# Performance work log

Hardware: AMD Instinct MI355X
Metric: run time of the kernel (lower is better)

Reference implementation:

```python
import jax, jax.numpy as jnp
import numpy as np

BN_EPS = 1e-5
TAU = 1.0

def _conv(x, w, pad, groups=1):
    return jax.lax.conv_general_dilated(
        x, w, (1, 1), [(pad, pad), (pad, pad)],
        feature_group_count=groups,
        dimension_numbers=('NCHW', 'OIHW', 'NCHW'))

def _bn(x, p):
    # p: (4, C) rows = gamma, beta, running_mean, running_var (eval-mode BN)
    g, b, m, v = p[0], p[1], p[2], p[3]
    scale = g * jax.lax.rsqrt(v + BN_EPS)
    shift = b - m * scale
    return x * scale[None, :, None, None] + shift[None, :, None, None]

def _dsconv(x, dw, bn1, pw, bn2, pad):
    c = x.shape[1]
    h = jax.nn.silu(_bn(_conv(x, dw, pad, groups=c), bn1))
    return jax.nn.silu(_bn(_conv(h, pw, 0), bn2))

def _make_bn(key, ch):
    k1, k2, k3, k4 = jax.random.split(key, 4)
    g = 1.0 + 0.1 * jax.random.normal(k1, (ch,), jnp.float32)
    b = 0.1 * jax.random.normal(k2, (ch,), jnp.float32)
    m = 0.1 * jax.random.normal(k3, (ch,), jnp.float32)
    v = 0.5 + jax.random.uniform(k4, (ch,), jnp.float32)
    return jnp.stack([g, b, m, v])

def setup_inputs() -> dict:
    key = jax.random.key(0)
    ks = jax.random.split(key, 18)
    B, C, H, W = 4, 256, 128, 128
    P, K = 64, 8
    inp = {
        'x':      jax.random.normal(ks[0], (B, C, H, W), jnp.float32),
        'fp_w1':  0.05 * jax.random.normal(ks[1], (P, C, 1, 1), jnp.float32),
        'fp_bn1': _make_bn(ks[2], P),
        'fp_dw':  0.2 * jax.random.normal(ks[3], (P, 1, 3, 3), jnp.float32),
        'fp_bn2': _make_bn(ks[4], P),
        'protos': jax.random.normal(ks[5], (K, P), jnp.float32),
        'bs_dw':  0.2 * jax.random.normal(ks[6], (1, 1, 3, 3), jnp.float32),
        'bs_bn1': _make_bn(ks[7], 1),
        'bs_pw':  0.2 * jax.random.normal(ks[8], (8, 1, 1, 1), jnp.float32),
        'bs_bn2': _make_bn(ks[9], 8),
        'bl_dw':  0.2 * jax.random.normal(ks[10], (1, 1, 5, 5), jnp.float32),
        'bl_bn1': _make_bn(ks[11], 1),
        'bl_pw':  0.2 * jax.random.normal(ks[12], (8, 1, 1, 1), jnp.float32),
        'bl_bn2': _make_bn(ks[13], 8),
        'fuse_w': 0.2 * jax.random.normal(ks[14], (1, 16, 1, 1), jnp.float32),
        'fuse_b': 0.1 * jax.random.normal(ks[15], (1,), jnp.float32),
        'gamma':  0.5 * jax.random.normal(ks[16], (1,), jnp.float32),
    }
    return inp

def reference(x, fp_w1, fp_bn1, fp_dw, fp_bn2, protos,
              bs_dw, bs_bn1, bs_pw, bs_bn2,
              bl_dw, bl_bn1, bl_pw, bl_bn2,
              fuse_w, fuse_b, gamma):
    # feature_proj: 1x1 conv -> BN -> SiLU -> depthwise 3x3 -> BN -> SiLU
    h = jax.nn.silu(_bn(_conv(x, fp_w1, 0), fp_bn1))
    proj = jax.nn.silu(_bn(_conv(h, fp_dw, 1, groups=fp_dw.shape[0]), fp_bn2))

    # deviation: min L2 distance to K bg prototypes, per-image min-max normalized
    B, P, H, W = proj.shape
    feat = proj.reshape(B, P, H * W).transpose(0, 2, 1)      # (B, HW, P)
    d2 = ((feat * feat).sum(-1, keepdims=True)               # (B, HW, 1)
          + (protos * protos).sum(-1)                        # (K,)
          - 2.0 * jnp.einsum('bnp,kp->bnk', feat, protos))   # (B, HW, K)
    dist = jnp.sqrt(jnp.maximum(d2, 0.0))
    min_dist = dist.min(axis=2) / (TAU + 1e-6)               # (B, HW)
    d_min = min_dist.min(axis=1, keepdims=True)
    d_max = min_dist.max(axis=1, keepdims=True)
    deviation = ((min_dist - d_min) / (d_max - d_min + 1e-6)).reshape(B, 1, H, W)

    # deviation -> attention head: two DS-conv branches (3x3 and 5x5), fuse 1x1, sigmoid
    f1 = _dsconv(deviation, bs_dw, bs_bn1, bs_pw, bs_bn2, pad=1)
    f2 = _dsconv(deviation, bl_dw, bl_bn1, bl_pw, bl_bn2, pad=2)
    attn = jax.nn.sigmoid(_conv(jnp.concatenate([f1, f2], axis=1), fuse_w, 0)
                          + fuse_b[None, :, None, None])
    return x + gamma * (x * attn)
```

## Files before the change

### kernel.cpp

```cpp
#include <hip/hip_runtime.h>
#include <math.h>

#define C_IN 256
#define P_CH 64
#define H_IMG 128
#define W_IMG 128
#define HW (H_IMG*W_IMG)
#define N_IMG 4
#define K_PROTO 8
#define BN_EPS 1e-5f

typedef unsigned short u16;
typedef __attribute__((ext_vector_type(4))) short bf16x4;
typedef __attribute__((ext_vector_type(8))) short bf16x8;
typedef __attribute__((ext_vector_type(4))) float f32x4;

#define OFF_WTBF   0
#define OFF_BIASA  8192
#define OFF_PNORM  8256
#define OFF_MINMAX 8264
#define OFF_H      8272
#define OFF_MD     (8272 + 2097152)
#define OFF_ATTN   (OFF_MD + 65536)

__device__ __forceinline__ float silu_f(float x) { return x / (1.f + __expf(-x)); }

__device__ __forceinline__ u16 f2bf(float f) {
    union { float f; unsigned u; } v; v.f = f;
    unsigned r = v.u + 0x7fffu + ((v.u >> 16) & 1u);
    return (u16)(r >> 16);
}
__device__ __forceinline__ float bf2f(u16 s) {
    union { unsigned u; float f; } v; v.u = ((unsigned)s) << 16; return v.f;
}

__global__ void prep_kernel(const float* __restrict__ w1, const float* __restrict__ bn1,
                            const float* __restrict__ protos, float* __restrict__ ws)
{
    int bx = blockIdx.x, tid = threadIdx.x;
    if (bx < 64) {
        int idx = bx * 256 + tid;
        int n = idx >> 8, k = idx & 255;
        float sc = bn1[n] * rsqrtf(bn1[192 + n] + BN_EPS);
        ((u16*)(ws + OFF_WTBF))[idx] = f2bf(w1[n * C_IN + k] * sc);
    } else {
        if (tid < 64) {
            float sc = bn1[tid] * rsqrtf(bn1[192 + tid] + BN_EPS);
            ws[OFF_BIASA + tid] = bn1[64 + tid] - bn1[128 + tid] * sc;
        }
        if (tid < 8) {
            float s = 0.f;
            for (int p = 0; p < 64; ++p) { float v = protos[tid * 64 + p]; s += v * v; }
            ws[OFF_PNORM + tid] = s;
        }
        if (tid < 4) {
            unsigned* mm = (unsigned*)(ws + OFF_MINMAX);
            mm[tid * 2]     = 0x7f7fffffu;
            mm[tid * 2 + 1] = 0u;
        }
    }
}

#define LDA 36
#define LDB 264
__global__ __launch_bounds__(256) void conv1x1_kernel(
    const float* __restrict__ x, const u16* __restrict__ wtb,
    const float* __restrict__ bias, u16* __restrict__ h)
{
    __shared__ u16 As[2][128 * LDA];
    __shared__ u16 Bs[64 * LDB];
    int bx = blockIdx.x;
    int img = bx >> 7, row = bx & 127;
    int tid = threadIdx.x;
    int wid = tid >> 6, lane = tid & 63;
    int mm = lane & 15, kb = lane >> 4;

    {
        int n = tid >> 2, k0 = (tid & 3) * 64;
        const u16* src = wtb + n * 256 + k0;
        u16* dst = Bs + n * LDB + k0;
#pragma unroll
        for (int i = 0; i < 64; i += 4)
            *(ushort4*)(dst + i) = *(const ushort4*)(src + i);
    }

    int cp = tid >> 4, pg = tid & 15;
    const float* xbase = x + (size_t)img * C_IN * HW + row * W_IMG;
    {
        const float* xc0 = xbase + (size_t)(2 * cp) * HW;
        const float* xc1 = xc0 + HW;
#pragma unroll
        for (int i = 0; i < 8; ++i) {
            int px = pg + 16 * i;
            ushort2 pk; pk.x = f2bf(xc0[px]); pk.y = f2bf(xc1[px]);
            *(ushort2*)(&As[0][px * LDA + 2 * cp]) = pk;
        }
    }
    __syncthreads();

    f32x4 acc[2][4];
#pragma unroll
    for (int mt = 0; mt < 2; ++mt)
#pragma unroll
        for (int nt = 0; nt < 4; ++nt) acc[mt][nt] = (f32x4){0.f, 0.f, 0.f, 0.f};

    for (int k = 0; k < 8; ++k) {
        float p0[8], p1[8];
        if (k < 7) {
            const float* xc0 = xbase + (size_t)((k + 1) * 32 + 2 * cp) * HW;
            const float* xc1 = xc0 + HW;
#pragma unroll
            for (int i = 0; i < 8; ++i) {
                int px = pg + 16 * i;
                p0[i] = xc0[px]; p1[i] = xc1[px];
            }
        }

        const u16* Ab = As[k & 1];
        bf16x8 afrag[2], bfrag[4];
#pragma unroll
        for (int mt = 0; mt < 2; ++mt) {
            const u16* ap = Ab + (wid * 32 + mt * 16 + mm) * LDA + kb * 8;
            bf16x4 lo = *(const bf16x4*)ap;
            bf16x4 hi = *(const bf16x4*)(ap + 4);
            afrag[mt] = __builtin_shufflevector(lo, hi, 0, 1, 2, 3, 4, 5, 6, 7);
        }
#pragma unroll
        for (int nt = 0; nt < 4; ++nt)
            bfrag[nt] = *(const bf16x8*)(Bs + (nt * 16 + mm) * LDB + k * 32 + kb * 8);
#pragma unroll
        for (int mt = 0; mt < 2; ++mt)
#pragma unroll
            for (int nt = 0; nt < 4; ++nt)
                acc[mt][nt] = __builtin_amdgcn_mfma_f32_16x16x32_bf16(
                    afrag[mt], bfrag[nt], acc[mt][nt], 0, 0, 0);

        if (k < 7) {
            u16* An = As[(k + 1) & 1];
#pragma unroll
            for (int i = 0; i < 8; ++i) {
                int px = pg + 16 * i;
                ushort2 pk; pk.x = f2bf(p0[i]); pk.y = f2bf(p1[i]);
                *(ushort2*)(&An[px * LDA + 2 * cp]) = pk;
            }
        }
        __syncthreads();
    }

#pragma unroll
    for (int mt = 0; mt < 2; ++mt) {
        int pxb = wid * 32 + mt * 16 + kb * 4;
#pragma unroll
        for (int nt = 0; nt < 4; ++nt) {
            int n = nt * 16 + mm;
            float bb = bias[n];
            ushort4 o;
            o.x = f2bf(silu_f(acc[mt][nt][0] + bb));
            o.y = f2bf(silu_f(acc[mt][nt][1] + bb));
            o.z = f2bf(silu_f(acc[mt][nt][2] + bb));
            o.w = f2bf(silu_f(acc[mt][nt][3] + bb));
            *(ushort4*)(h + ((size_t)img * P_CH + n) * HW + row * W_IMG + pxb) = o;
        }
    }
}

__global__ __launch_bounds__(1024) void dwconv_dev_kernel(
    const u16* __restrict__ h, const float* __restrict__ dw,
    const float* __restrict__ bn2, const float* __restrict__ protos,
    const float* __restrict__ pnorm, float* __restrict__ md,
    unsigned* __restrict__ minmax)
{
    __shared__ float smem[4 * 8 * 324];
    int img = blockIdx.x >> 6;
    int t = blockIdx.x & 63;
    int y0 = (t >> 3) << 4, x0 = (t & 7) << 4;
    int tid = threadIdx.x;
    int q = tid >> 8;
    int qtid = tid & 255;
    int ty = qtid >> 4, tx = qtid & 15;

    const u16* himg = h + (size_t)img * P_CH * HW;
    float* qt = smem + q * (8 * 324);

    int  pre_off[11];
    bool pre_ok[11];
    bool pre_v[11];
#pragma unroll
    for (int r = 0; r < 11; ++r) {
        int l = qtid + r * 256;
        bool valid = l < 2592;
        int cl = l / 324;
        int rr = l - cl * 324;
        int ly = rr / 18, lx = rr - ly * 18;
        int yy = y0 - 1 + ly, xx = x0 - 1 + lx;
        bool inb = (yy >= 0) & (yy < H_IMG) & (xx >= 0) & (xx < W_IMG);
        pre_v[r] = valid;
        pre_ok[r] = valid && inb;
        pre_off[r] = cl * HW + (inb ? (yy * W_IMG + xx) : 0);
    }

    float norm2 = 0.f;
    float dot[K_PROTO];
#pragma unroll
    for (int k = 0; k < K_PROTO; ++k) dot[k] = 0.f;

    {
        const u16* hs = himg + (size_t)(q * 16) * HW;
#pragma unroll
        for (int r = 0; r < 11; ++r) {
            float v = pre_ok[r] ? bf2f(hs[pre_off[r]]) : 0.f;
            if (pre_v[r]) qt[qtid + r * 256] = v;
        }
    }
    __syncthreads();

    for (int k = 0; k < 2; ++k) {
        float pf[11];
        if (k == 0) {
            const u16* hs = himg + (size_t)(q * 16 + 8) * HW;
#pragma unroll
            for (int r = 0; r < 11; ++r)
                pf[r] = pre_ok[r] ? bf2f(hs[pre_off[r]]) : 0.f;
        }

        int c0 = q * 16 + k * 8;
#pragma unroll
        for (int cl = 0; cl < 8; ++cl) {
            int ch = c0 + cl;
            const float* tc = qt + cl * 324;
            const float* wch = dw + ch * 9;
            float s = 0.f;
#pragma unroll
            for (int dy = 0; dy < 3; ++dy)
#pragma unroll
                for (int dx = 0; dx < 3; ++dx)
                    s = fmaf(tc[(ty + dy) * 18 + tx + dx], wch[dy * 3 + dx], s);
            float g = bn2[ch], bb = bn2[64 + ch], m = bn2[128 + ch], vv = bn2[192 + ch];
            float scale = g * rsqrtf(vv + BN_EPS);
            float val = silu_f(scale * s + (bb - m * scale));
            norm2 = fmaf(val, val, norm2);
#pragma unroll
            for (int kk = 0; kk < K_PROTO; ++kk)
                dot[kk] = fmaf(val, protos[kk * 64 + ch], dot[kk]);
        }

        if (k == 0) {
            __syncthreads();
#pragma unroll
            for (int r = 0; r < 11; ++r)
                if (pre_v[r]) qt[qtid + r * 256] = pf[r];
            __syncthreads();
        }
    }
    __syncthreads();

    float* P = smem;
    {
        float* dst = P + (q * 256 + qtid) * 9;
        dst[0] = norm2;
#pragma unroll
        for (int kk = 0; kk < K_PROTO; ++kk) dst[1 + kk] = dot[kk];
    }
    __syncthreads();

    float wmin = 1e30f, wmax = -1e30f, mdv = 0.f;
    if (q == 0) {
        float n2 = 0.f, dd[K_PROTO];
#pragma unroll
        for (int kk = 0; kk < K_PROTO; ++kk) dd[kk] = 0.f;
#pragma unroll
        for (int qq = 0; qq < 4; ++qq) {
            const float* src = P + (qq * 256 + qtid) * 9;
            n2 += src[0];
#pragma unroll
            for (int kk = 0; kk < K_PROTO; ++kk) dd[kk] += src[1 + kk];
        }
        float d2min = 1e30f;
#pragma unroll
        for (int kk = 0; kk < K_PROTO; ++kk)
            d2min = fminf(d2min, n2 + pnorm[kk] - 2.f * dd[kk]);
        mdv = sqrtf(fmaxf(d2min, 0.f)) * (1.f / 1.000001f);
        md[img * HW + (y0 + ty) * W_IMG + (x0 + tx)] = mdv;
        wmin = mdv; wmax = mdv;
#pragma unroll
        for (int d = 32; d > 0; d >>= 1) {
            wmin = fminf(wmin, __shfl_xor(wmin, d));
            wmax = fmaxf(wmax, __shfl_xor(wmax, d));
        }
    }
    __syncthreads();
    if (q == 0 && (qtid & 63) == 0) {
        int wid = qtid >> 6;
        smem[wid * 2]     = wmin;
        smem[wid * 2 + 1] = wmax;
    }
    __syncthreads();
    if (tid == 0) {
        float bmin = fminf(fminf(smem[0], smem[2]), fminf(smem[4], smem[6]));
        float bmax = fmaxf(fmaxf(smem[1], smem[3]), fmaxf(smem[5], smem[7]));
        atomicMin(&minmax[img * 2],     __float_as_uint(bmin));
        atomicMax(&minmax[img * 2 + 1], __float_as_uint(bmax));
    }
}

__global__ __launch_bounds__(256) void attn_kernel(
    const float* __restrict__ md, const unsigned* __restrict__ minmax,
    const float* __restrict__ bs_dw, const float* __restrict__ bs_bn1,
    const float* __restrict__ bs_pw, const float* __restrict__ bs_bn2,
    const float* __restrict__ bl_dw, const float* __restrict__ bl_bn1,
    const float* __restrict__ bl_pw, const float* __restrict__ bl_bn2,
    const float* __restrict__ fuse_w, const float* __restrict__ fuse_b,
    float* __restrict__ attn)
{
    __shared__ float tile[20 * 20];
    int img = blockIdx.x >> 6;
    int t = blockIdx.x & 63;
    int y0 = (t >> 3) << 4, x0 = (t & 7) << 4;
    int tid = threadIdx.x;
    int ty = tid >> 4, tx = tid & 15;

    float fdmin = __uint_as_float(minmax[img * 2]);
    float fdmax = __uint_as_float(minmax[img * 2 + 1]);
    float inv = 1.f / (fdmax - fdmin + 1e-6f);

    const float* mdi = md + img * HW;
    for (int l = tid; l < 400; l += 256) {
        int ly = l / 20, lx = l - ly * 20;
        int yy = y0 - 2 + ly, xx = x0 - 2 + lx;
        float v = 0.f;
        if (yy >= 0 && yy < H_IMG && xx >= 0 && xx < W_IMG)
            v = (mdi[yy * W_IMG + xx] - fdmin) * inv;
        tile[l] = v;
    }
    __syncthreads();

    float c3 = 0.f;
#pragma unroll
    for (int dy = 0; dy < 3; ++dy)
#pragma unroll
        for (int dx = 0; dx < 3; ++dx)
            c3 = fmaf(tile[(ty + 1 + dy) * 20 + tx + 1 + dx], bs_dw[dy * 3 + dx], c3);
    float c5 = 0.f;
#pragma unroll
    for (int dy = 0; dy < 5; ++dy)
#pragma unroll
        for (int dx = 0; dx < 5; ++dx)
            c5 = fmaf(tile[(ty + dy) * 20 + tx + dx], bl_dw[dy * 5 + dx], c5);

    float s1 = bs_bn1[0] * rsqrtf(bs_bn1[3] + BN_EPS);
    float t1 = silu_f(s1 * c3 + (bs_bn1[1] - bs_bn1[2] * s1));
    float s2 = bl_bn1[0] * rsqrtf(bl_bn1[3] + BN_EPS);
    float t2 = silu_f(s2 * c5 + (bl_bn1[1] - bl_bn1[2] * s2));

    float acc = fuse_b[0];
#pragma unroll
    for (int c = 0; c < 8; ++c) {
        float scs = bs_bn2[c] * rsqrtf(bs_bn2[24 + c] + BN_EPS);
        float u1 = silu_f(scs * (bs_pw[c] * t1) + (bs_bn2[8 + c] - bs_bn2[16 + c] * scs));
        acc = fmaf(fuse_w[c], u1, acc);
        float scl = bl_bn2[c] * rsqrtf(bl_bn2[24 + c] + BN_EPS);
        float u2 = silu_f(scl * (bl_pw[c] * t2) + (bl_bn2[8 + c] - bl_bn2[16 + c] * scl));
        acc = fmaf(fuse_w[8 + c], u2, acc);
    }
    float a = 1.f / (1.f + __expf(-acc));
    attn[img * HW + (y0 + ty) * W_IMG + (x0 + tx)] = a;
}

__global__ __launch_bounds__(256) void final_kernel(
    const float* __restrict__ x, const float* __restrict__ attn,
    const float* __restrict__ gamma, float* __restrict__ out)
{
    size_t i = ((size_t)blockIdx.x * 256 + (size_t)threadIdx.x) * 4;
    float g = gamma[0];
    int b = (int)(i / ((size_t)C_IN * HW));
    int hw = (int)(i % HW);
    const float4 xv = *(const float4*)(x + i);
    const float4 av = *(const float4*)(attn + (size_t)b * HW + hw);
    float4 o;
    o.x = xv.x * (1.f + g * av.x);
    o.y = xv.y * (1.f + g * av.y);
    o.z = xv.z * (1.f + g * av.z);
    o.w = xv.w * (1.f + g * av.w);
    *(float4*)(out + i) = o;
}

extern "C" void kernel_launch(void* const* d_in, const int* in_sizes, int n_in,
                              void* d_out, int out_size, void* d_ws, size_t ws_size,
                              hipStream_t stream) {
    const float* x      = (const float*)d_in[0];
    const float* fp_w1  = (const float*)d_in[1];
    const float* fp_bn1 = (const float*)d_in[2];
    const float* fp_dw  = (const float*)d_in[3];
    const float* fp_bn2 = (const float*)d_in[4];
    const float* protos = (const float*)d_in[5];
    const float* bs_dw  = (const float*)d_in[6];
    const float* bs_bn1 = (const float*)d_in[7];
    const float* bs_pw  = (const float*)d_in[8];
    const float* bs_bn2 = (const float*)d_in[9];
    const float* bl_dw  = (const float*)d_in[10];
    const float* bl_bn1 = (const float*)d_in[11];
    const float* bl_pw  = (const float*)d_in[12];
    const float* bl_bn2 = (const float*)d_in[13];
    const float* fuse_w = (const float*)d_in[14];
    const float* fuse_b = (const float*)d_in[15];
    const float* gamma  = (const float*)d_in[16];
    float* ws  = (float*)d_ws;
    float* out = (float*)d_out;

    prep_kernel<<<65, 256, 0, stream>>>(fp_w1, fp_bn1, protos, ws);
    conv1x1_kernel<<<512, 256, 0, stream>>>(x, (const u16*)(ws + OFF_WTBF),
                                            ws + OFF_BIASA, (u16*)(ws + OFF_H));
    dwconv_dev_kernel<<<256, 1024, 0, stream>>>((const u16*)(ws + OFF_H), fp_dw, fp_bn2,
                                                protos, ws + OFF_PNORM, ws + OFF_MD,
                                                (unsigned*)(ws + OFF_MINMAX));
    attn_kernel<<<256, 256, 0, stream>>>(ws + OFF_MD, (const unsigned*)(ws + OFF_MINMAX),
                                         bs_dw, bs_bn1, bs_pw, bs_bn2,
                                         bl_dw, bl_bn1, bl_pw, bl_bn2,
                                         fuse_w, fuse_b, ws + OFF_ATTN);
    final_kernel<<<16384, 256, 0, stream>>>(x, ws + OFF_ATTN, gamma, out);
}
```

Before: 188.9 us.

## Fuse 1x1 conv GEMM with depthwise conv and prototype distance via halo tiles

Merges the bf16 MFMA 1x1 projection and the depthwise 3x3 + prototype-distance kernels into one kernel that works on 16x8 pixel tiles with a one-pixel halo. The projected features stay in shared memory, so the intermediate h tensor is no longer written to and read back from global memory. The cost is recomputing the GEMM on halo pixels (180 of 192 padded rows per tile for 128 outputs) and more gather-like loads of x with boundary masks. A-tile double buffering is dropped in favour of a single buffer with extra barriers, and min/max reductions are adjusted to the new tile layout.

After: 221.5 us. +17.3%, slower.

```diff
diff --git a/kernel.cpp b/kernel.cpp
--- a/kernel.cpp
+++ b/kernel.cpp
@@ -19,8 +19,7 @@
 #define OFF_BIASA  8192
 #define OFF_PNORM  8256
 #define OFF_MINMAX 8264
-#define OFF_H      8272
-#define OFF_MD     (8272 + 2097152)
+#define OFF_MD     8272
 #define OFF_ATTN   (OFF_MD + 65536)
 
 __device__ __forceinline__ float silu_f(float x) { return x / (1.f + __expf(-x)); }
@@ -61,16 +60,30 @@
     }
 }
 
-#define LDA 36
-#define LDB 264
-__global__ __launch_bounds__(256) void conv1x1_kernel(
+#define HALO_PX 180
+#define M_PAD   192
+#define LDA     36
+#define LDB     264
+#define LDH     200
+__global__ __launch_bounds__(256, 2) void fused_front_kernel(
     const float* __restrict__ x, const u16* __restrict__ wtb,
-    const float* __restrict__ bias, u16* __restrict__ h)
+    const float* __restrict__ biasA, const float* __restrict__ dw,
+    const float* __restrict__ bn2, const float* __restrict__ protos,
+    const float* __restrict__ pnorm, float* __restrict__ md,
+    unsigned* __restrict__ minmax)
 {
-    __shared__ u16 As[2][128 * LDA];
-    __shared__ u16 Bs[64 * LDB];
+    __shared__ unsigned long long smem8[47616 / 8];
+    u16* Bs = (u16*)smem8;
+    u16* As = Bs + 64 * LDB;
+    u16* Hs = (u16*)smem8;
+    float* Pp = (float*)((char*)smem8 + 25600);
+    float* mmx = (float*)((char*)smem8 + 30208);
+
     int bx = blockIdx.x;
-    int img = bx >> 7, row = bx & 127;
+    int img = bx >> 7;
+    int t = bx & 127;
+    int ty0 = (t >> 4) << 4;
+    int tx0 = (t & 15) << 3;
     int tid = threadIdx.x;
     int wid = tid >> 6, lane = tid & 63;
     int mm = lane & 15, kb = lane >> 4;
@@ -83,44 +96,64 @@
         for (int i = 0; i < 64; i += 4)
             *(ushort4*)(dst + i) = *(const ushort4*)(src + i);
     }
+    if (tid < 216) ((unsigned*)(As + HALO_PX * LDA))[tid] = 0u;
 
     int cp = tid >> 4, pg = tid & 15;
-    const float* xbase = x + (size_t)img * C_IN * HW + row * W_IMG;
+    int off[12];
+    unsigned wm = 0, vm = 0;
+#pragma unroll
+    for (int i = 0; i < 12; ++i) {
+        int p = pg + 16 * i;
+        int y = (p * 205) >> 11;
+        int xx = p - y * 10;
+        int gy = ty0 - 1 + y, gx = tx0 - 1 + xx;
+        bool w = p < HALO_PX;
+        bool v = w && gy >= 0 && gy < H_IMG && gx >= 0 && gx < W_IMG;
+        if (w) wm |= 1u << i;
+        if (v) vm |= 1u << i;
+        off[i] = v ? (gy * W_IMG + gx) : 0;
+    }
+    const float* xim = x + (size_t)img * C_IN * HW;
+
+    float f0[12], f1[12];
     {
-        const float* xc0 = xbase + (size_t)(2 * cp) * HW;
+        const float* xc0 = xim + (size_t)(2 * cp) * HW;
         const float* xc1 = xc0 + HW;
 #pragma unroll
-        for (int i = 0; i < 8; ++i) {
-            int px = pg + 16 * i;
-            ushort2 pk; pk.x = f2bf(xc0[px]); pk.y = f2bf(xc1[px]);
-            *(ushort2*)(&As[0][px * LDA + 2 * cp]) = pk;
-        }
-    }
-    __syncthreads();
-
-    f32x4 acc[2][4];
-#pragma unroll
-    for (int mt = 0; mt < 2; ++mt)
+        for (int i = 0; i < 12; ++i) {
+            f0[i] = (vm >> i & 1) ? xc0[off[i]] : 0.f;
+            f1[i] = (vm >> i & 1) ? xc1[off[i]] : 0.f;
+        }
+#pragma unroll
+        for (int i = 0; i < 12; ++i)
+            if (wm >> i & 1) {
+                ushort2 pk; pk.x = f2bf(f0[i]); pk.y = f2bf(f1[i]);
+                *(ushort2*)&As[(pg + 16 * i) * LDA + 2 * cp] = pk;
+            }
+    }
+    __syncthreads();
+
+    f32x4 acc[3][4];
+#pragma unroll
+    for (int mt = 0; mt < 3; ++mt)
 #pragma unroll
         for (int nt = 0; nt < 4; ++nt) acc[mt][nt] = (f32x4){0.f, 0.f, 0.f, 0.f};
 
     for (int k = 0; k < 8; ++k) {
-        float p0[8], p1[8];
         if (k < 7) {
-            const float* xc0 = xbase + (size_t)((k + 1) * 32 + 2 * cp) * HW;
+            const float* xc0 = xim + (size_t)((k + 1) * 32 + 2 * cp) * HW;
             const float* xc1 = xc0 + HW;
 #pragma unroll
-            for (int i = 0; i < 8; ++i) {
-                int px = pg + 16 * i;
-                p0[i] = xc0[px]; p1[i] = xc1[px];
+            for (int i = 0; i < 12; ++i) {
+                f0[i] = (vm >> i & 1) ? xc0[off[i]] : 0.f;
+                f1[i] = (vm >> i & 1) ? xc1[off[i]] : 0.f;
             }
         }
 
-        const u16* Ab = As[k & 1];
-        bf16x8 afrag[2], bfrag[4];
-#pragma unroll
-        for (int mt = 0; mt < 2; ++mt) {
-            const u16* ap = Ab + (wid * 32 + mt * 16 + mm) * LDA + kb * 8;
+        bf16x8 afrag[3], bfrag[4];
+#pragma unroll
+        for (int mt = 0; mt < 3; ++mt) {
+            const u16* ap = As + ((wid * 3 + mt) * 16 + mm) * LDA + kb * 8;
             bf16x4 lo = *(const bf16x4*)ap;
             bf16x4 hi = *(const bf16x4*)(ap + 4);
             afrag[mt] = __builtin_shufflevector(lo, hi, 0, 1, 2, 3, 4, 5, 6, 7);
@@ -129,175 +162,115 @@
         for (int nt = 0; nt < 4; ++nt)
             bfrag[nt] = *(const bf16x8*)(Bs + (nt * 16 + mm) * LDB + k * 32 + kb * 8);
 #pragma unroll
-        for (int mt = 0; mt < 2; ++mt)
+        for (int mt = 0; mt < 3; ++mt)
 #pragma unroll
             for (int nt = 0; nt < 4; ++nt)
                 acc[mt][nt] = __builtin_amdgcn_mfma_f32_16x16x32_bf16(
                     afrag[mt], bfrag[nt], acc[mt][nt], 0, 0, 0);
+        __syncthreads();
 
         if (k < 7) {
-            u16* An = As[(k + 1) & 1];
-#pragma unroll
-            for (int i = 0; i < 8; ++i) {
-                int px = pg + 16 * i;
-                ushort2 pk; pk.x = f2bf(p0[i]); pk.y = f2bf(p1[i]);
-                *(ushort2*)(&An[px * LDA + 2 * cp]) = pk;
-            }
-        }
-        __syncthreads();
-    }
-
-#pragma unroll
-    for (int mt = 0; mt < 2; ++mt) {
-        int pxb = wid * 32 + mt * 16 + kb * 4;
+#pragma unroll
+            for (int i = 0; i < 12; ++i)
+                if (wm >> i & 1) {
+                    ushort2 pk; pk.x = f2bf(f0[i]); pk.y = f2bf(f1[i]);
+                    *(ushort2*)&As[(pg + 16 * i) * LDA + 2 * cp] = pk;
+                }
+            __syncthreads();
+        }
+    }
+
+    float biasv[4];
+#pragma unroll
+    for (int nt = 0; nt < 4; ++nt) biasv[nt] = biasA[nt * 16 + mm];
+#pragma unroll
+    for (int mt = 0; mt < 3; ++mt) {
+        int p0 = (wid * 3 + mt) * 16 + kb * 4;
+        bool pv[4];
+#pragma unroll
+        for (int r = 0; r < 4; ++r) {
+            int p = p0 + r;
+            int y = (p * 205) >> 11;
+            int xx = p - y * 10;
+            int gy = ty0 - 1 + y, gx = tx0 - 1 + xx;
+            pv[r] = (p < HALO_PX) && gy >= 0 && gy < H_IMG && gx >= 0 && gx < W_IMG;
+        }
 #pragma unroll
         for (int nt = 0; nt < 4; ++nt) {
             int n = nt * 16 + mm;
-            float bb = bias[n];
             ushort4 o;
-            o.x = f2bf(silu_f(acc[mt][nt][0] + bb));
-            o.y = f2bf(silu_f(acc[mt][nt][1] + bb));
-            o.z = f2bf(silu_f(acc[mt][nt][2] + bb));
-            o.w = f2bf(silu_f(acc[mt][nt][3] + bb));
-            *(ushort4*)(h + ((size_t)img * P_CH + n) * HW + row * W_IMG + pxb) = o;
-        }
-    }
-}
-
-__global__ __launch_bounds__(1024) void dwconv_dev_kernel(
-    const u16* __restrict__ h, const float* __restrict__ dw,
-    const float* __restrict__ bn2, const float* __restrict__ protos,
-    const float* __restrict__ pnorm, float* __restrict__ md,
-    unsigned* __restrict__ minmax)
-{
-    __shared__ float smem[4 * 8 * 324];
-    int img = blockIdx.x >> 6;
-    int t = blockIdx.x & 63;
-    int y0 = (t >> 3) << 4, x0 = (t & 7) << 4;
-    int tid = threadIdx.x;
-    int q = tid >> 8;
-    int qtid = tid & 255;
-    int ty = qtid >> 4, tx = qtid & 15;
-
-    const u16* himg = h + (size_t)img * P_CH * HW;
-    float* qt = smem + q * (8 * 324);
-
-    int  pre_off[11];
-    bool pre_ok[11];
-    bool pre_v[11];
-#pragma unroll
-    for (int r = 0; r < 11; ++r) {
-        int l = qtid + r * 256;
-        bool valid = l < 2592;
-        int cl = l / 324;
-        int rr = l - cl * 324;
-        int ly = rr / 18, lx = rr - ly * 18;
-        int yy = y0 - 1 + ly, xx = x0 - 1 + lx;
-        bool inb = (yy >= 0) & (yy < H_IMG) & (xx >= 0) & (xx < W_IMG);
-        pre_v[r] = valid;
-        pre_ok[r] = valid && inb;
-        pre_off[r] = cl * HW + (inb ? (yy * W_IMG + xx) : 0);
-    }
+            o.x = pv[0] ? f2bf(silu_f(acc[mt][nt][0] + biasv[nt])) : (u16)0;
+            o.y = pv[1] ? f2bf(silu_f(acc[mt][nt][1] + biasv[nt])) : (u16)0;
+            o.z = pv[2] ? f2bf(silu_f(acc[mt][nt][2] + biasv[nt])) : (u16)0;
+            o.w = pv[3] ? f2bf(silu_f(acc[mt][nt][3] + biasv[nt])) : (u16)0;
+            *(ushort4*)&Hs[n * LDH + p0] = o;
+        }
+    }
+    __syncthreads();
+
+    int half = tid >> 7, pxl = tid & 127;
+    int oy = pxl >> 3, ox = pxl & 7;
+    int pb = oy * 10 + ox;
 
     float norm2 = 0.f;
     float dot[K_PROTO];
 #pragma unroll
-    for (int k = 0; k < K_PROTO; ++k) dot[k] = 0.f;
-
-    {
-        const u16* hs = himg + (size_t)(q * 16) * HW;
-#pragma unroll
-        for (int r = 0; r < 11; ++r) {
-            float v = pre_ok[r] ? bf2f(hs[pre_off[r]]) : 0.f;
-            if (pre_v[r]) qt[qtid + r * 256] = v;
-        }
-    }
-    __syncthreads();
-
-    for (int k = 0; k < 2; ++k) {
-        float pf[11];
-        if (k == 0) {
-            const u16* hs = himg + (size_t)(q * 16 + 8) * HW;
-#pragma unroll
-            for (int r = 0; r < 11; ++r)
-                pf[r] = pre_ok[r] ? bf2f(hs[pre_off[r]]) : 0.f;
-        }
-
-        int c0 = q * 16 + k * 8;
-#pragma unroll
-        for (int cl = 0; cl < 8; ++cl) {
-            int ch = c0 + cl;
-            const float* tc = qt + cl * 324;
-            const float* wch = dw + ch * 9;
-            float s = 0.f;
-#pragma unroll
-            for (int dy = 0; dy < 3; ++dy)
-#pragma unroll
-                for (int dx = 0; dx < 3; ++dx)
-                    s = fmaf(tc[(ty + dy) * 18 + tx + dx], wch[dy * 3 + dx], s);
-            float g = bn2[ch], bb = bn2[64 + ch], m = bn2[128 + ch], vv = bn2[192 + ch];
-            float scale = g * rsqrtf(vv + BN_EPS);
-            float val = silu_f(scale * s + (bb - m * scale));
-            norm2 = fmaf(val, val, norm2);
-#pragma unroll
-            for (int kk = 0; kk < K_PROTO; ++kk)
-                dot[kk] = fmaf(val, protos[kk * 64 + ch], dot[kk]);
-        }
-
-        if (k == 0) {
-            __syncthreads();
-#pragma unroll
-            for (int r = 0; r < 11; ++r)
-                if (pre_v[r]) qt[qtid + r * 256] = pf[r];
-            __syncthreads();
-        }
-    }
-    __syncthreads();
-
-    float* P = smem;
-    {
-        float* dst = P + (q * 256 + qtid) * 9;
-        dst[0] = norm2;
-#pragma unroll
-        for (int kk = 0; kk < K_PROTO; ++kk) dst[1 + kk] = dot[kk];
-    }
-    __syncthreads();
-
-    float wmin = 1e30f, wmax = -1e30f, mdv = 0.f;
-    if (q == 0) {
-        float n2 = 0.f, dd[K_PROTO];
-#pragma unroll
-        for (int kk = 0; kk < K_PROTO; ++kk) dd[kk] = 0.f;
-#pragma unroll
-        for (int qq = 0; qq < 4; ++qq) {
-            const float* src = P + (qq * 256 + qtid) * 9;
-            n2 += src[0];
-#pragma unroll
-            for (int kk = 0; kk < K_PROTO; ++kk) dd[kk] += src[1 + kk];
-        }
+    for (int kk = 0; kk < K_PROTO; ++kk) dot[kk] = 0.f;
+
+    for (int cl = 0; cl < 32; ++cl) {
+        int ch = half * 32 + cl;
+        const u16* hc = Hs + ch * LDH;
+        const float* wch = dw + ch * 9;
+        float s = 0.f;
+#pragma unroll
+        for (int dy = 0; dy < 3; ++dy)
+#pragma unroll
+            for (int dx = 0; dx < 3; ++dx)
+                s = fmaf(bf2f(hc[pb + dy * 10 + dx]), wch[dy * 3 + dx], s);
+        float g = bn2[ch], bb = bn2[64 + ch], m = bn2[128 + ch], vv = bn2[192 + ch];
+        float scale = g * rsqrtf(vv + BN_EPS);
+        float val = silu_f(scale * s + (bb - m * scale));
+        norm2 = fmaf(val, val, norm2);
+#pragma unroll
+        for (int kk = 0; kk < K_PROTO; ++kk)
+            dot[kk] = fmaf(val, protos[kk * 64 + ch], dot[kk]);
+    }
+
+    if (half == 1) {
+        float* d = Pp + pxl * 9;
+        d[0] = norm2;
+#pragma unroll
+        for (int kk = 0; kk < K_PROTO; ++kk) d[1 + kk] = dot[kk];
+    }
+    __syncthreads();
+
+    if (half == 0) {
+        const float* sadd = Pp + pxl * 9;
+        norm2 += sadd[0];
+#pragma unroll
+        for (int kk = 0; kk < K_PROTO; ++kk) dot[kk] += sadd[1 + kk];
         float d2min = 1e30f;
 #pragma unroll
         for (int kk = 0; kk < K_PROTO; ++kk)
-            d2min = fminf(d2min, n2 + pnorm[kk] - 2.f * dd[kk]);
-        mdv = sqrtf(fmaxf(d2min, 0.f)) * (1.f / 1.000001f);
-        md[img * HW + (y0 + ty) * W_IMG + (x0 + tx)] = mdv;
-        wmin = mdv; wmax = mdv;
+            d2min = fminf(d2min, norm2 + pnorm[kk] - 2.f * dot[kk]);
+        float mdv = sqrtf(fmaxf(d2min, 0.f)) * (1.f / 1.000001f);
+        md[img * HW + (ty0 + oy) * W_IMG + (tx0 + ox)] = mdv;
+
+        float wmin = mdv, wmax = mdv;
 #pragma unroll
         for (int d = 32; d > 0; d >>= 1) {
             wmin = fminf(wmin, __shfl_xor(wmin, d));
             wmax = fmaxf(wmax, __shfl_xor(wmax, d));
         }
-    }
-    __syncthreads();
-    if (q == 0 && (qtid & 63) == 0) {
-        int wid = qtid >> 6;
-        smem[wid * 2]     = wmin;
-        smem[wid * 2 + 1] = wmax;
+        if (lane == 0) {
+            mmx[wid * 2]     = wmin;
+            mmx[wid * 2 + 1] = wmax;
+        }
     }
     __syncthreads();
     if (tid == 0) {
-        float bmin = fminf(fminf(smem[0], smem[2]), fminf(smem[4], smem[6]));
-        float bmax = fmaxf(fmaxf(smem[1], smem[3]), fmaxf(smem[5], smem[7]));
+        float bmin = fminf(mmx[0], mmx[2]);
+        float bmax = fmaxf(mmx[1], mmx[3]);
         atomicMin(&minmax[img * 2],     __float_as_uint(bmin));
         atomicMax(&minmax[img * 2 + 1], __float_as_uint(bmax));
     }
@@ -408,10 +381,9 @@
     float* out = (float*)d_out;
 
     prep_kernel<<<65, 256, 0, stream>>>(fp_w1, fp_bn1, protos, ws);
-    conv1x1_kernel<<<512, 256, 0, stream>>>(x, (const u16*)(ws + OFF_WTBF),
-                                            ws + OFF_BIASA, (u16*)(ws + OFF_H));
-    dwconv_dev_kernel<<<256, 1024, 0, stream>>>((const u16*)(ws + OFF_H), fp_dw, fp_bn2,
-                                                protos, ws + OFF_PNORM, ws + OFF_MD,
+    fused_front_kernel<<<512, 256, 0, stream>>>(x, (const u16*)(ws + OFF_WTBF),
+                                                ws + OFF_BIASA, fp_dw, fp_bn2, protos,
+                                                ws + OFF_PNORM, ws + OFF_MD,
                                                 (unsigned*)(ws + OFF_MINMAX));
     attn_kernel<<<256, 256, 0, stream>>>(ws + OFF_MD, (const unsigned*)(ws + OFF_MINMAX),
                                          bs_dw, bs_bn1, bs_pw, bs_bn2,
```
